# Kernel tuning notes

Hardware: AMD Instinct MI355X
Metric: run time of the kernel (lower is better)

## Reference

```python
import jax, jax.numpy as jnp
import numpy as np
import math

# ---- module hyperparameters (match init_kwargs) ----
B = 2            # batch
CTX = 512        # context_length
C = 16           # n_subspaces
RS = 16          # rank_subspace
RT = 16          # rank_transformations
T = 2 + 2 * RT   # 34 transformation slots
L = int(math.isqrt(CTX * C * 2))  # latent_dim = 128
K = int(math.isqrt(L))            # 11
H, W = 1024, 1024                 # output_shape
EPS = 1e-12


def siglog(x):
    # dyna.functional.siglog: sign(x) * log(1 + |x|)
    return jnp.sign(x) * jnp.log1p(jnp.abs(x))


def linear_interp_last(x, out_size):
    """F.interpolate(mode='linear', align_corners=False) along last axis."""
    in_size = x.shape[-1]
    scale = in_size / out_size
    pos = (jnp.arange(out_size, dtype=jnp.float32) + 0.5) * scale - 0.5
    pos = jnp.clip(pos, 0.0, in_size - 1)
    i0 = jnp.floor(pos).astype(jnp.int32)
    i1 = jnp.minimum(i0 + 1, in_size - 1)
    w = (pos - i0.astype(jnp.float32)).astype(x.dtype)
    return x[..., i0] * (1.0 - w) + x[..., i1] * w


def setup_inputs() -> dict:
    key = jax.random.key(0)
    ks = jax.random.split(key, 8)
    x = jax.random.normal(ks[0], (B, CTX), dtype=jnp.float32)
    # nn.Linear(CTX, L*4): store weight as [in, out]
    W_ctx = jax.random.normal(ks[1], (CTX, L * 4), dtype=jnp.float32) / np.sqrt(CTX)
    b_ctx = jax.random.normal(ks[2], (L * 4,), dtype=jnp.float32) * 0.01
    space_i = jax.random.normal(ks[3], (1, C, RS, H, 2), dtype=jnp.float32)
    space_j = jax.random.normal(ks[4], (1, C, RS, W, 2), dtype=jnp.float32)
    # xavier-ish scale for the CP factors
    gA = np.sqrt(2.0 / (L + K))
    A = jax.random.normal(ks[5], (T, C, L, K, RS, 2), dtype=jnp.float32) * gA
    Bf = jax.random.normal(ks[6], (T, C, K, L, RS, 2), dtype=jnp.float32) * gA
    return {"x": x, "W_ctx": W_ctx, "b_ctx": b_ctx, "A": A, "Bf": Bf,
            "space_i": space_i, "space_j": space_j}


def _apply_space(space, shift, z, size):
    # space: [1,C,RS,size,2]; shift: [B,C,RS,2]; z: [B,RT,C,RS,2]
    sp = space + shift[:, :, :, None, :]                     # [B,C,RS,size,2]
    z = jnp.transpose(z, (0, 4, 2, 3, 1))                    # [B,2,C,RS,RT]
    z = linear_interp_last(z, size)                          # [B,2,C,RS,size]
    z = jnp.transpose(z, (0, 2, 3, 4, 1))                    # [B,C,RS,size,2]
    prod = sp * z
    re = prod[..., 1:] - prod[..., :1]                       # diff over last dim (size 2)
    im = (sp * z[..., ::-1]).sum(axis=-1, keepdims=True)     # a0*z1 + a1*z0
    return jnp.concatenate([re, im], axis=-1)                # [B,C,RS,size,2]


def reference(x, W_ctx, b_ctx, A, Bf, space_i, space_j):
    # context transform + siglog modulation
    xt = x @ W_ctx + b_ctx                                   # [B, 4L]
    s = 2 * L
    xm = (xt[:, :s] * siglog(xt[:, s:])).reshape(-1, L, 2)   # [B,L,2]
    xr, xi = xm[..., 0], xm[..., 1]                          # [B,L]

    # Complex broadcast einsums: i = x * A (btclki), j = x * B (btclkj).
    # (i*j).sum(k) == x^2 * sum_k(A[t,c,l,k,r] * B[t,c,k,l,r])  (complex)
    Ar, Ai = A[..., 0], A[..., 1]                            # [T,C,L,K,RS]
    Br, Bi = Bf[..., 0], Bf[..., 1]                          # [T,C,K,L,RS]
    ABr = jnp.einsum('tclkr,tcklr->tclr', Ar, Br) - jnp.einsum('tclkr,tcklr->tclr', Ai, Bi)
    ABi = jnp.einsum('tclkr,tcklr->tclr', Ar, Bi) + jnp.einsum('tclkr,tcklr->tclr', Ai, Br)
    x2r = xr * xr - xi * xi                                  # [B,L]
    x2i = 2.0 * xr * xi
    x2r_b = x2r[:, None, None, :, None]                      # [B,1,1,L,1]
    x2i_b = x2i[:, None, None, :, None]
    Re = x2r_b * ABr[None] - x2i_b * ABi[None]               # [B,T,C,L,RS]
    Im = x2r_b * ABi[None] + x2i_b * ABr[None]

    # polar normalization + magnitude-weighted averaging over L (dim 3)
    mag = jnp.sqrt(Re * Re + Im * Im + EPS)
    cos_t = Re / mag
    sin_t = Im / mag
    msum = mag.sum(axis=3)
    cosw = (cos_t * mag).sum(axis=3) / (msum + EPS)          # [B,T,C,RS]
    sinw = (sin_t * mag).sum(axis=3) / (msum + EPS)
    mag_mean = mag.mean(axis=3)
    tr = jnp.stack([cosw * mag_mean, sinw * mag_mean], axis=-1)  # [B,T,C,RS,2]

    out_i = _apply_space(space_i, tr[:, 0], tr[:, 2:2 + RT], H)
    out_j = _apply_space(space_j, tr[:, 1], tr[:, 2 + RT:2 + 2 * RT], W)
    return out_i, out_j
```

## Files before the change

### kernel.cpp

```cpp
#include <hip/hip_runtime.h>
#include <math.h>

#define B_   2
#define CTX_ 512
#define C_   16
#define RS_  16
#define RT_  16
#define T_   34
#define L_   128
#define K_   11
#define H_   1024
#define EPS_ 1e-12f

__device__ __forceinline__ float siglog(float v) {
    return copysignf(log1pf(fabsf(v)), v);
}

__global__ __launch_bounds__(512) void k_ctx(const float* __restrict__ x,
                                             const float* __restrict__ Wc,
                                             const float* __restrict__ bc,
                                             float2* __restrict__ x2out) {
    __shared__ float xrow[CTX_];
    __shared__ float xt[4 * L_];
    const int b = blockIdx.x;
    const int tid = threadIdx.x;
    xrow[tid] = x[b * CTX_ + tid];
    __syncthreads();
    float sum = bc[tid];
#pragma unroll 8
    for (int c = 0; c < CTX_; ++c)
        sum = fmaf(xrow[c], Wc[c * (4 * L_) + tid], sum);
    xt[tid] = sum;
    __syncthreads();
    if (tid < L_) {
        float xr = xt[2 * tid]     * siglog(xt[2 * L_ + 2 * tid]);
        float xi = xt[2 * tid + 1] * siglog(xt[2 * L_ + 2 * tid + 1]);
        x2out[b * L_ + tid] = make_float2(xr * xr - xi * xi, 2.0f * xr * xi);
    }
}

__global__ __launch_bounds__(256) void k_tr(const float2* __restrict__ A2,
                                            const float2* __restrict__ B2,
                                            const float2* __restrict__ x2,
                                            float2* __restrict__ tr2) {
    const int blk = blockIdx.x;
    const int tid = threadIdx.x;
    const int r  = tid & 15;
    const int lg = tid >> 4;

    __shared__ float sxr[B_][L_];
    __shared__ float sxi[B_][L_];
    {
        float2 v = x2[tid];
        sxr[tid >> 7][tid & 127] = v.x;
        sxi[tid >> 7][tid & 127] = v.y;
    }
    __syncthreads();

    const float2* __restrict__ Ab = A2 + (size_t)blk * (L_ * K_ * RS_);
    const float2* __restrict__ Bb = B2 + (size_t)blk * (K_ * L_ * RS_);

    float sRe[B_] = {0.f, 0.f}, sIm[B_] = {0.f, 0.f}, sM[B_] = {0.f, 0.f};

    for (int j = 0; j < L_ / 16; ++j) {
        const int l = lg + 16 * j;
        float abr = 0.f, abi = 0.f;
#pragma unroll
        for (int k = 0; k < K_; ++k) {
            float2 a  = Ab[(l * K_ + k) * RS_ + r];
            float2 bv = Bb[(k * L_ + l) * RS_ + r];
            abr = fmaf(a.x, bv.x, abr);
            abr = fmaf(-a.y, bv.y, abr);
            abi = fmaf(a.x, bv.y, abi);
            abi = fmaf(a.y, bv.x, abi);
        }
#pragma unroll
        for (int b = 0; b < B_; ++b) {
            float xr2 = sxr[b][l], xi2 = sxi[b][l];
            float Re = xr2 * abr - xi2 * abi;
            float Im = xr2 * abi + xi2 * abr;
            float mag = sqrtf(fmaf(Re, Re, fmaf(Im, Im, EPS_)));
            sRe[b] += Re; sIm[b] += Im; sM[b] += mag;
        }
    }

    __shared__ float red[16][16][6];
    red[lg][r][0] = sRe[0]; red[lg][r][1] = sIm[0]; red[lg][r][2] = sM[0];
    red[lg][r][3] = sRe[1]; red[lg][r][4] = sIm[1]; red[lg][r][5] = sM[1];
    __syncthreads();

    if (tid < 2 * RS_) {
        const int b = tid >> 4, rr = tid & 15;
        float a0 = 0.f, a1 = 0.f, a2 = 0.f;
#pragma unroll
        for (int g = 0; g < 16; ++g) {
            a0 += red[g][rr][b * 3 + 0];
            a1 += red[g][rr][b * 3 + 1];
            a2 += red[g][rr][b * 3 + 2];
        }
        const float inv = a2 / ((a2 + EPS_) * (float)L_);
        const int t = blk / C_, c = blk % C_;
        tr2[(((size_t)b * T_ + t) * C_ + c) * RS_ + rr] = make_float2(a0 * inv, a1 * inv);
    }
}

__global__ __launch_bounds__(256) void k_out(const float2* __restrict__ space_i,
                                             const float2* __restrict__ space_j,
                                             const float2* __restrict__ tr2,
                                             float2* __restrict__ out) {
    const int half = B_ * C_ * RS_ * H_;
    int idx = blockIdx.x * blockDim.x + threadIdx.x;
    if (idx >= 2 * half) return;
    const int which = (idx >= half) ? 1 : 0;
    int id = idx - which * half;

    const int h = id & (H_ - 1);
    int rest = id >> 10;
    const int r = rest & 15; rest >>= 4;
    const int c = rest & 15;
    const int b = rest >> 4;

    const float2* __restrict__ sp2 = which ? space_j : space_i;

    const size_t trb = (((size_t)b * T_) * C_ + c) * RS_ + r;
    const size_t trs = (size_t)C_ * RS_;

    const float2 sh = tr2[trb + (size_t)which * trs];

    float pos = (h + 0.5f) * (16.0f / 1024.0f) - 0.5f;
    pos = fminf(fmaxf(pos, 0.0f), 15.0f);
    const int i0 = (int)floorf(pos);
    const int i1 = min(i0 + 1, RT_ - 1);
    const float w = pos - (float)i0;

    const int tb = 2 + which * RT_;
    const float2 z0 = tr2[trb + (size_t)(tb + i0) * trs];
    const float2 z1 = tr2[trb + (size_t)(tb + i1) * trs];
    const float zx = z0.x * (1.0f - w) + z1.x * w;
    const float zy = z0.y * (1.0f - w) + z1.y * w;

    const float2 sv = sp2[((size_t)c * RS_ + r) * H_ + h];
    const float sx = sv.x + sh.x;
    const float sy = sv.y + sh.y;

    out[idx] = make_float2(sy * zy - sx * zx, sx * zy + sy * zx);
}

extern "C" void kernel_launch(void* const* d_in, const int* in_sizes, int n_in,
                              void* d_out, int out_size, void* d_ws, size_t ws_size,
                              hipStream_t stream) {
    const float*  x  = (const float*)d_in[0];
    const float*  Wc = (const float*)d_in[1];
    const float*  bc = (const float*)d_in[2];
    const float2* A2 = (const float2*)d_in[3];
    const float2* B2 = (const float2*)d_in[4];
    const float2* si = (const float2*)d_in[5];
    const float2* sj = (const float2*)d_in[6];

    float2* x2  = (float2*)d_ws;
    float2* tr2 = (float2*)((char*)d_ws + 4096);

    k_ctx<<<B_, 512, 0, stream>>>(x, Wc, bc, x2);
    k_tr<<<T_ * C_, 256, 0, stream>>>(A2, B2, x2, tr2);

    const int total = 2 * B_ * C_ * RS_ * H_;
    k_out<<<(total + 255) / 256, 256, 0, stream>>>(si, sj, tr2, (float2*)d_out);
}
```

Measured before the change: 66.44 us.

## Split transformation reduction across L chunks with vectorized loads and finalize kernel

The per-(t,c) transformation kernel is split into four blocks per slot, each handling 32 of the 128 latent positions. Each thread now loads float4 values covering two rank entries and reduces with wave shuffles, and partial sums go to a workspace buffer. A new small kernel combines the partials and applies the normalization. The change exposes more parallelism (2176 blocks instead of 544) and widens memory accesses, at the cost of an extra kernel launch and a partial-sum round trip through global memory.

```diff
diff --git a/kernel.cpp b/kernel.cpp
--- a/kernel.cpp
+++ b/kernel.cpp
@@ -11,6 +11,9 @@
 #define K_   11
 #define H_   1024
 #define EPS_ 1e-12f
+
+#define NSPLIT_ 4
+#define LCHUNK_ 32
 
 __device__ __forceinline__ float siglog(float v) {
     return copysignf(log1pf(fabsf(v)), v);
@@ -39,69 +42,99 @@
     }
 }
 
-__global__ __launch_bounds__(256) void k_tr(const float2* __restrict__ A2,
-                                            const float2* __restrict__ B2,
-                                            const float2* __restrict__ x2,
-                                            float2* __restrict__ tr2) {
+__global__ __launch_bounds__(256) void k_tr_part(const float4* __restrict__ A4,
+                                                 const float4* __restrict__ B4,
+                                                 const float2* __restrict__ x2,
+                                                 float* __restrict__ part) {
     const int blk = blockIdx.x;
+    const int tc  = blk / NSPLIT_;
+    const int s   = blk % NSPLIT_;
     const int tid = threadIdx.x;
-    const int r  = tid & 15;
-    const int lg = tid >> 4;
-
-    __shared__ float sxr[B_][L_];
-    __shared__ float sxi[B_][L_];
-    {
-        float2 v = x2[tid];
-        sxr[tid >> 7][tid & 127] = v.x;
-        sxi[tid >> 7][tid & 127] = v.y;
+    const int rp  = tid & 7;
+    const int l   = s * LCHUNK_ + (tid >> 3);
+
+    const float4* __restrict__ Ab = A4 + ((size_t)(tc * L_ + l) * K_) * 8 + rp;
+    const float4* __restrict__ Bb = B4 + ((size_t)tc * K_ * L_ + l) * 8 + rp;
+
+    float abr0 = 0.f, abi0 = 0.f, abr1 = 0.f, abi1 = 0.f;
+#pragma unroll
+    for (int k = 0; k < K_; ++k) {
+        float4 a  = Ab[(size_t)k * 8];
+        float4 bv = Bb[(size_t)k * L_ * 8];
+        abr0 = fmaf(a.x, bv.x, abr0); abr0 = fmaf(-a.y, bv.y, abr0);
+        abi0 = fmaf(a.x, bv.y, abi0); abi0 = fmaf( a.y, bv.x, abi0);
+        abr1 = fmaf(a.z, bv.z, abr1); abr1 = fmaf(-a.w, bv.w, abr1);
+        abi1 = fmaf(a.z, bv.w, abi1); abi1 = fmaf( a.w, bv.z, abi1);
+    }
+
+    float acc[12];
+#pragma unroll
+    for (int b = 0; b < B_; ++b) {
+        float2 xv = x2[b * L_ + l];
+        float Re0 = xv.x * abr0 - xv.y * abi0;
+        float Im0 = xv.x * abi0 + xv.y * abr0;
+        float Re1 = xv.x * abr1 - xv.y * abi1;
+        float Im1 = xv.x * abi1 + xv.y * abr1;
+        acc[b * 6 + 0] = Re0;
+        acc[b * 6 + 1] = Im0;
+        acc[b * 6 + 2] = sqrtf(fmaf(Re0, Re0, fmaf(Im0, Im0, EPS_)));
+        acc[b * 6 + 3] = Re1;
+        acc[b * 6 + 4] = Im1;
+        acc[b * 6 + 5] = sqrtf(fmaf(Re1, Re1, fmaf(Im1, Im1, EPS_)));
+    }
+
+#pragma unroll
+    for (int off = 8; off <= 32; off <<= 1) {
+#pragma unroll
+        for (int i = 0; i < 12; ++i)
+            acc[i] += __shfl_xor(acc[i], off);
+    }
+
+    __shared__ float wred[4][8][12];
+    const int wave = tid >> 6;
+    const int lane = tid & 63;
+    if (lane < 8) {
+#pragma unroll
+        for (int i = 0; i < 12; ++i) wred[wave][lane][i] = acc[i];
     }
     __syncthreads();
 
-    const float2* __restrict__ Ab = A2 + (size_t)blk * (L_ * K_ * RS_);
-    const float2* __restrict__ Bb = B2 + (size_t)blk * (K_ * L_ * RS_);
-
-    float sRe[B_] = {0.f, 0.f}, sIm[B_] = {0.f, 0.f}, sM[B_] = {0.f, 0.f};
-
-    for (int j = 0; j < L_ / 16; ++j) {
-        const int l = lg + 16 * j;
-        float abr = 0.f, abi = 0.f;
-#pragma unroll
-        for (int k = 0; k < K_; ++k) {
-            float2 a  = Ab[(l * K_ + k) * RS_ + r];
-            float2 bv = Bb[(k * L_ + l) * RS_ + r];
-            abr = fmaf(a.x, bv.x, abr);
-            abr = fmaf(-a.y, bv.y, abr);
-            abi = fmaf(a.x, bv.y, abi);
-            abi = fmaf(a.y, bv.x, abi);
-        }
-#pragma unroll
-        for (int b = 0; b < B_; ++b) {
-            float xr2 = sxr[b][l], xi2 = sxi[b][l];
-            float Re = xr2 * abr - xi2 * abi;
-            float Im = xr2 * abi + xi2 * abr;
-            float mag = sqrtf(fmaf(Re, Re, fmaf(Im, Im, EPS_)));
-            sRe[b] += Re; sIm[b] += Im; sM[b] += mag;
-        }
-    }
-
-    __shared__ float red[16][16][6];
-    red[lg][r][0] = sRe[0]; red[lg][r][1] = sIm[0]; red[lg][r][2] = sM[0];
-    red[lg][r][3] = sRe[1]; red[lg][r][4] = sIm[1]; red[lg][r][5] = sM[1];
-    __syncthreads();
-
-    if (tid < 2 * RS_) {
-        const int b = tid >> 4, rr = tid & 15;
-        float a0 = 0.f, a1 = 0.f, a2 = 0.f;
-#pragma unroll
-        for (int g = 0; g < 16; ++g) {
-            a0 += red[g][rr][b * 3 + 0];
-            a1 += red[g][rr][b * 3 + 1];
-            a2 += red[g][rr][b * 3 + 2];
-        }
-        const float inv = a2 / ((a2 + EPS_) * (float)L_);
-        const int t = blk / C_, c = blk % C_;
-        tr2[(((size_t)b * T_ + t) * C_ + c) * RS_ + rr] = make_float2(a0 * inv, a1 * inv);
-    }
+    if (tid < 96) {
+        const int rp2  = tid >> 2;
+    }
+    if (tid < 96) {
+        const int rpi  = tid / 12;
+        const int comp = tid % 12;
+        float v = wred[0][rpi][comp] + wred[1][rpi][comp]
+                + wred[2][rpi][comp] + wred[3][rpi][comp];
+        const int b    = comp / 6;
+        const int pair = (comp / 3) & 1;
+        const int c3   = comp % 3;
+        const int r    = 2 * rpi + pair;
+        part[(((size_t)blk * B_ + b) * RS_ + r) * 3 + c3] = v;
+    }
+}
+
+__global__ __launch_bounds__(256) void k_tr_fin(const float* __restrict__ part,
+                                                float2* __restrict__ tr2) {
+    const int idx = blockIdx.x * blockDim.x + threadIdx.x;
+    const int total = T_ * C_ * B_ * RS_;
+    if (idx >= total) return;
+    const int r  = idx & 15;
+    const int b  = (idx >> 4) & 1;
+    const int tc = idx >> 5;
+
+    float a0 = 0.f, a1 = 0.f, a2 = 0.f;
+#pragma unroll
+    for (int s = 0; s < NSPLIT_; ++s) {
+        const size_t base = (((size_t)(tc * NSPLIT_ + s) * B_ + b) * RS_ + r) * 3;
+        a0 += part[base + 0];
+        a1 += part[base + 1];
+        a2 += part[base + 2];
+    }
+    const float inv = a2 / ((a2 + EPS_) * (float)L_);
+    const int t = tc / C_, c = tc % C_;
+    tr2[(((size_t)b * T_ + t) * C_ + c) * RS_ + r] = make_float2(a0 * inv, a1 * inv);
 }
 
 __global__ __launch_bounds__(256) void k_out(const float2* __restrict__ space_i,
@@ -152,16 +185,21 @@
     const float*  x  = (const float*)d_in[0];
     const float*  Wc = (const float*)d_in[1];
     const float*  bc = (const float*)d_in[2];
-    const float2* A2 = (const float2*)d_in[3];
-    const float2* B2 = (const float2*)d_in[4];
+    const float4* A4 = (const float4*)d_in[3];
+    const float4* B4 = (const float4*)d_in[4];
     const float2* si = (const float2*)d_in[5];
     const float2* sj = (const float2*)d_in[6];
 
-    float2* x2  = (float2*)d_ws;
-    float2* tr2 = (float2*)((char*)d_ws + 4096);
+    float2* x2   = (float2*)d_ws;
+    float*  part = (float*)((char*)d_ws + 4096);
+    float2* tr2  = (float2*)((char*)d_ws + 4096 + 1024 * 1024);
 
     k_ctx<<<B_, 512, 0, stream>>>(x, Wc, bc, x2);
-    k_tr<<<T_ * C_, 256, 0, stream>>>(A2, B2, x2, tr2);
+
+    k_tr_part<<<T_ * C_ * NSPLIT_, 256, 0, stream>>>(A4, B4, x2, part);
+
+    const int fin_total = T_ * C_ * B_ * RS_;
+    k_tr_fin<<<(fin_total + 255) / 256, 256, 0, stream>>>(part, tr2);
 
     const int total = 2 * B_ * C_ * RS_ * H_;
     k_out<<<(total + 255) / 256, 256, 0, stream>>>(si, sj, tr2, (float2*)d_out);
```

Result: no change. 66.06 us (-0.6%).

## Split transformation reduction into pipelined LDS-staged chunks with atomic partials

Applied to the files above, without the earlier changes.

Replaces the per-(t,c) reduction kernel with a persistent-style kernel of 512 blocks, each handling 17 chunks of 8 L-rows. A and B factors are staged into a triple-buffered LDS ring with async global_load_lds, and the next chunk's loads overlap compute on the current one. Partial sums are combined via wave shuffles and global atomics, then finalized by a separate small kernel. This spreads the A/B streaming over more blocks to raise bandwidth, at the cost of an extra memset, an extra launch, atomic traffic, and only two of four waves computing.

```diff
diff --git a/kernel.cpp b/kernel.cpp
--- a/kernel.cpp
+++ b/kernel.cpp
@@ -12,8 +12,23 @@
 #define H_   1024
 #define EPS_ 1e-12f
 
+#define NSPLIT_  16
+#define LCHUNK_  8
+#define NCHUNK_  (T_ * C_ * NSPLIT_)
+#define NBLK_    512
+#define NCHPB_   17
+#define CHUNKB_  (LCHUNK_ * K_ * 128)
+#define NLOAD_   22
+#define NBUF_    3
+
 __device__ __forceinline__ float siglog(float v) {
     return copysignf(log1pf(fabsf(v)), v);
+}
+
+__device__ __forceinline__ void gload_lds16(const void* g, void* l) {
+    __builtin_amdgcn_global_load_lds(
+        (const __attribute__((address_space(1))) unsigned int*)g,
+        (__attribute__((address_space(3))) unsigned int*)l, 16, 0, 0);
 }
 
 __global__ __launch_bounds__(512) void k_ctx(const float* __restrict__ x,
@@ -39,69 +54,123 @@
     }
 }
 
-__global__ __launch_bounds__(256) void k_tr(const float2* __restrict__ A2,
-                                            const float2* __restrict__ B2,
-                                            const float2* __restrict__ x2,
-                                            float2* __restrict__ tr2) {
-    const int blk = blockIdx.x;
-    const int tid = threadIdx.x;
-    const int r  = tid & 15;
-    const int lg = tid >> 4;
-
-    __shared__ float sxr[B_][L_];
-    __shared__ float sxi[B_][L_];
-    {
-        float2 v = x2[tid];
-        sxr[tid >> 7][tid & 127] = v.x;
-        sxi[tid >> 7][tid & 127] = v.y;
-    }
-    __syncthreads();
-
-    const float2* __restrict__ Ab = A2 + (size_t)blk * (L_ * K_ * RS_);
-    const float2* __restrict__ Bb = B2 + (size_t)blk * (K_ * L_ * RS_);
-
-    float sRe[B_] = {0.f, 0.f}, sIm[B_] = {0.f, 0.f}, sM[B_] = {0.f, 0.f};
-
-    for (int j = 0; j < L_ / 16; ++j) {
-        const int l = lg + 16 * j;
-        float abr = 0.f, abi = 0.f;
-#pragma unroll
-        for (int k = 0; k < K_; ++k) {
-            float2 a  = Ab[(l * K_ + k) * RS_ + r];
-            float2 bv = Bb[(k * L_ + l) * RS_ + r];
-            abr = fmaf(a.x, bv.x, abr);
-            abr = fmaf(-a.y, bv.y, abr);
-            abi = fmaf(a.x, bv.y, abi);
-            abi = fmaf(a.y, bv.x, abi);
-        }
-#pragma unroll
-        for (int b = 0; b < B_; ++b) {
-            float xr2 = sxr[b][l], xi2 = sxi[b][l];
-            float Re = xr2 * abr - xi2 * abi;
-            float Im = xr2 * abi + xi2 * abr;
-            float mag = sqrtf(fmaf(Re, Re, fmaf(Im, Im, EPS_)));
-            sRe[b] += Re; sIm[b] += Im; sM[b] += mag;
+__device__ __forceinline__ void stage_chunk(const char* __restrict__ Ag,
+                                            const char* __restrict__ Bg,
+                                            int ch, char* dA, char* dB,
+                                            int wave, int lane) {
+    const int tc = ch >> 4, s = ch & 15;
+    const char* Ab = Ag + (size_t)(tc * L_ + s * LCHUNK_) * (K_ * 128);
+    const char* Bb = Bg + (size_t)tc * (K_ * L_ * 128) + (size_t)s * (LCHUNK_ * 128);
+    for (int id = wave; id < NLOAD_; id += 4) {
+        if (id < K_) {
+            gload_lds16(Ab + id * 1024 + lane * 16, dA + id * 1024);
+        } else {
+            const int k = id - K_;
+            gload_lds16(Bb + (size_t)k * (L_ * 128) + lane * 16, dB + k * 1024);
         }
     }
-
-    __shared__ float red[16][16][6];
-    red[lg][r][0] = sRe[0]; red[lg][r][1] = sIm[0]; red[lg][r][2] = sM[0];
-    red[lg][r][3] = sRe[1]; red[lg][r][4] = sIm[1]; red[lg][r][5] = sM[1];
-    __syncthreads();
-
-    if (tid < 2 * RS_) {
-        const int b = tid >> 4, rr = tid & 15;
-        float a0 = 0.f, a1 = 0.f, a2 = 0.f;
+}
+
+__global__ __launch_bounds__(256) void k_tr_part(const char* __restrict__ Ag,
+                                                 const char* __restrict__ Bg,
+                                                 const float2* __restrict__ x2g,
+                                                 float* __restrict__ part) {
+    __shared__ __attribute__((aligned(16))) char bufA[NBUF_][CHUNKB_];
+    __shared__ __attribute__((aligned(16))) char bufB[NBUF_][CHUNKB_];
+    __shared__ float2 x2s[B_ * L_];
+
+    const int tid  = threadIdx.x;
+    const int wave = tid >> 6;
+    const int lane = tid & 63;
+    const int bk   = blockIdx.x;
+    const int r    = lane & 15;
+
+    x2s[tid] = x2g[tid];
+    asm volatile("s_waitcnt lgkmcnt(0)" ::: "memory");
+
+    stage_chunk(Ag, Bg, bk, bufA[0], bufB[0], wave, lane);
+
+    int cur = 0;
+    for (int i = 0; i < NCHPB_; ++i) {
+        const int nxt = (cur + 1 == NBUF_) ? 0 : cur + 1;
+
+        if (i + 1 < NCHPB_) {
+            stage_chunk(Ag, Bg, bk + (i + 1) * NBLK_, bufA[nxt], bufB[nxt], wave, lane);
+            __builtin_amdgcn_sched_barrier(0);
+            if (wave < 2) asm volatile("s_waitcnt vmcnt(6)" ::: "memory");
+            else          asm volatile("s_waitcnt vmcnt(5)" ::: "memory");
+        } else {
+            asm volatile("s_waitcnt vmcnt(0)" ::: "memory");
+        }
+        __builtin_amdgcn_sched_barrier(0);
+        __builtin_amdgcn_s_barrier();
+        __builtin_amdgcn_sched_barrier(0);
+
+        const int ch = bk + i * NBLK_;
+        const int tc = ch >> 4, s = ch & 15;
+
+        if (wave < 2) {
+            const int l = wave * 4 + (lane >> 4);
+            const float2* Al = (const float2*)&bufA[cur][(size_t)l * (K_ * 128)];
+            const float2* Bl = (const float2*)&bufB[cur][(size_t)l * 128];
+            float abr = 0.f, abi = 0.f;
 #pragma unroll
-        for (int g = 0; g < 16; ++g) {
-            a0 += red[g][rr][b * 3 + 0];
-            a1 += red[g][rr][b * 3 + 1];
-            a2 += red[g][rr][b * 3 + 2];
+            for (int k = 0; k < K_; ++k) {
+                float2 a  = Al[k * 16 + r];
+                float2 bv = Bl[k * 128 + r];
+                abr = fmaf(a.x, bv.x, abr); abr = fmaf(-a.y, bv.y, abr);
+                abi = fmaf(a.x, bv.y, abi); abi = fmaf( a.y, bv.x, abi);
+            }
+            const int lg = s * LCHUNK_ + l;
+            const float2 xv0 = x2s[lg];
+            const float2 xv1 = x2s[L_ + lg];
+            float acc[6];
+            {
+                float Re = xv0.x * abr - xv0.y * abi;
+                float Im = xv0.x * abi + xv0.y * abr;
+                acc[0] = Re; acc[1] = Im;
+                acc[2] = sqrtf(fmaf(Re, Re, fmaf(Im, Im, EPS_)));
+                Re = xv1.x * abr - xv1.y * abi;
+                Im = xv1.x * abi + xv1.y * abr;
+                acc[3] = Re; acc[4] = Im;
+                acc[5] = sqrtf(fmaf(Re, Re, fmaf(Im, Im, EPS_)));
+            }
+#pragma unroll
+            for (int j = 0; j < 6; ++j) acc[j] += __shfl_xor(acc[j], 16);
+#pragma unroll
+            for (int j = 0; j < 6; ++j) acc[j] += __shfl_xor(acc[j], 32);
+
+            if (lane < 16) {
+                float* p0 = &part[(((size_t)tc * B_ + 0) * RS_ + r) * 3];
+                float* p1 = &part[(((size_t)tc * B_ + 1) * RS_ + r) * 3];
+                atomicAdd(p0 + 0, acc[0]);
+                atomicAdd(p0 + 1, acc[1]);
+                atomicAdd(p0 + 2, acc[2]);
+                atomicAdd(p1 + 0, acc[3]);
+                atomicAdd(p1 + 1, acc[4]);
+                atomicAdd(p1 + 2, acc[5]);
+            }
         }
-        const float inv = a2 / ((a2 + EPS_) * (float)L_);
-        const int t = blk / C_, c = blk % C_;
-        tr2[(((size_t)b * T_ + t) * C_ + c) * RS_ + rr] = make_float2(a0 * inv, a1 * inv);
+        cur = nxt;
     }
+}
+
+__global__ __launch_bounds__(256) void k_tr_fin(const float* __restrict__ part,
+                                                float2* __restrict__ tr2) {
+    const int idx = blockIdx.x * blockDim.x + threadIdx.x;
+    const int total = T_ * C_ * B_ * RS_;
+    if (idx >= total) return;
+    const int r  = idx & 15;
+    const int b  = (idx >> 4) & 1;
+    const int tc = idx >> 5;
+
+    const size_t base = (((size_t)tc * B_ + b) * RS_ + r) * 3;
+    const float a0 = part[base + 0];
+    const float a1 = part[base + 1];
+    const float a2 = part[base + 2];
+    const float inv = a2 / ((a2 + EPS_) * (float)L_);
+    const int t = tc / C_, c = tc % C_;
+    tr2[(((size_t)b * T_ + t) * C_ + c) * RS_ + r] = make_float2(a0 * inv, a1 * inv);
 }
 
 __global__ __launch_bounds__(256) void k_out(const float2* __restrict__ space_i,
@@ -149,19 +218,27 @@
 extern "C" void kernel_launch(void* const* d_in, const int* in_sizes, int n_in,
                               void* d_out, int out_size, void* d_ws, size_t ws_size,
                               hipStream_t stream) {
-    const float*  x  = (const float*)d_in[0];
-    const float*  Wc = (const float*)d_in[1];
-    const float*  bc = (const float*)d_in[2];
-    const float2* A2 = (const float2*)d_in[3];
-    const float2* B2 = (const float2*)d_in[4];
+    const float* x  = (const float*)d_in[0];
+    const float* Wc = (const float*)d_in[1];
+    const float* bc = (const float*)d_in[2];
+    const char*  Ag = (const char*)d_in[3];
+    const char*  Bg = (const char*)d_in[4];
     const float2* si = (const float2*)d_in[5];
     const float2* sj = (const float2*)d_in[6];
 
-    float2* x2  = (float2*)d_ws;
-    float2* tr2 = (float2*)((char*)d_ws + 4096);
+    float2* x2   = (float2*)d_ws;
+    float*  part = (float*)((char*)d_ws + 4096);
+    float2* tr2  = (float2*)((char*)d_ws + 4096 + 256 * 1024);
+
+    const size_t part_bytes = (size_t)T_ * C_ * B_ * RS_ * 3 * sizeof(float);
+    hipMemsetAsync(part, 0, part_bytes, stream);
 
     k_ctx<<<B_, 512, 0, stream>>>(x, Wc, bc, x2);
-    k_tr<<<T_ * C_, 256, 0, stream>>>(A2, B2, x2, tr2);
+
+    k_tr_part<<<NBLK_, 256, 0, stream>>>(Ag, Bg, x2, part);
+
+    const int fin_total = T_ * C_ * B_ * RS_;
+    k_tr_fin<<<(fin_total + 255) / 256, 256, 0, stream>>>(part, tr2);
 
     const int total = 2 * B_ * C_ * RS_ * H_;
     k_out<<<(total + 255) / 256, 256, 0, stream>>>(si, sj, tr2, (float2*)d_out);
```

After: 77.15 us. 1.16x slower.
